# Performance work log

Measured on AMD Instinct MI355X. Metric: run time of the kernel, lower is better.

Reference implementation:

```python
import jax, jax.numpy as jnp
import numpy as np

B, N, C, H = 2, 1024, 1024, 16
D = C // H  # head_dim = 64

def _layernorm(x, g, b):
    m = jnp.mean(x, axis=-1, keepdims=True)
    v = jnp.mean((x - m) ** 2, axis=-1, keepdims=True)
    return (x - m) * jax.lax.rsqrt(v + 1e-5) * g + b

def _proj(x, w, b, g, beta):
    # Linear(C -> 2C) + LayerNorm(2C) + ReLU
    return jax.nn.relu(_layernorm(x @ w + b, g, beta))

def setup_inputs():
    key = jax.random.key(0)
    ks = jax.random.split(key, 9)
    mk = lambda k, shape, s=0.02: jax.random.normal(k, shape, dtype=jnp.float32) * s
    inp = {"x": jax.random.normal(ks[0], (B, N, C), dtype=jnp.float32)}
    for i, name in enumerate(["q", "k", "v"]):
        inp[name + "_w"] = mk(ks[1 + i], (C, 2 * C))
        inp[name + "_b"] = jnp.zeros((2 * C,), jnp.float32)
        inp[name + "_g"] = jnp.ones((2 * C,), jnp.float32)
        inp[name + "_beta"] = jnp.zeros((2 * C,), jnp.float32)
    inp["amp_mix"] = jax.random.normal(ks[7], (H,), dtype=jnp.float32)
    inp["phase_mix"] = jax.random.normal(ks[8], (H,), dtype=jnp.float32)
    return inp

def reference(x, q_w, q_b, q_g, q_beta, k_w, k_b, k_g, k_beta, v_w, v_b, v_g, v_beta, amp_mix, phase_mix):
    q = _proj(x, q_w, q_b, q_g, q_beta).reshape(B, N, H, 2 * D)
    k = _proj(x, k_w, k_b, k_g, k_beta).reshape(B, N, H, 2 * D)
    v = _proj(x, v_w, v_b, v_g, v_beta).reshape(B, N, H, 2 * D)
    qr, qi = q[..., :D], q[..., D:]
    kr, ki = k[..., :D], k[..., D:]
    vr, vi = v[..., :D], v[..., D:]
    # complex qk^H style logits: [B, N, M, H]
    amp = (jnp.einsum('bnhd,bmhd->bnmh', qr, kr)
           - jnp.einsum('bnhd,bmhd->bnmh', qi, ki)) * amp_mix
    ph = (jnp.einsum('bnhd,bmhd->bnmh', qr, ki)
          + jnp.einsum('bnhd,bmhd->bnmh', qi, kr)) * phase_mix
    # attn = amp * exp(i*ph); score = Re * sigmoid(Im)
    score = (amp * jnp.cos(ph)) * jax.nn.sigmoid(amp * jnp.sin(ph))
    attn = jax.nn.softmax(score, axis=2)  # softmax over keys (m)
    out_r = jnp.einsum('bnmh,bmhd->bnhd', attn, vr)
    out_i = jnp.einsum('bnmh,bmhd->bnhd', attn, vi)
    return jnp.concatenate([out_r, out_i], axis=-1).reshape(B, N, 2 * C)
```

## Files before the change

kernel.cpp:

```cpp
#include <hip/hip_runtime.h>
#include <math.h>

#define NSEQ   1024
#define KDIM   1024
#define TWOC   2048
#define NB     65536

typedef float  f32x4  __attribute__((ext_vector_type(4)));
typedef short  short8 __attribute__((ext_vector_type(8)));
typedef short  short4v __attribute__((ext_vector_type(4)));
typedef unsigned int u32x4 __attribute__((ext_vector_type(4)));
typedef __bf16 bf16x8 __attribute__((ext_vector_type(8)));
typedef _Float16 half8 __attribute__((ext_vector_type(8)));

#define PANROW   40
#define PANHALF  10240
#define PANPAIR  20480
#define NPAN_K   32
#define WPAN_Z_BYTES 10485760u

#define QPLANE   131072
#define KPLANEB  278528
#define VPLANEB  262144

#define QPAN_OFF   0ul
#define KPAN_OFF   16777216ul
#define VTPAN_OFF  34603008ul
#define QBUF_OFF   51380224ul
#define KBUF_OFF   68157440ul
#define VBUF_OFF   84934656ul

__device__ __forceinline__ unsigned short bf16_rne(float x) {
    unsigned int u = __float_as_uint(x);
    u += 0x7fffu + ((u >> 16) & 1u);
    return (unsigned short)(u >> 16);
}

__device__ __forceinline__ void gload_lds16(const void* g, void* l) {
    __builtin_amdgcn_global_load_lds(
        (const __attribute__((address_space(1))) unsigned int*)g,
        (__attribute__((address_space(3))) unsigned int*)l, 16, 0, 0);
}

__device__ __forceinline__ bf16x8 bneg(bf16x8 v) {
    u32x4 u = __builtin_bit_cast(u32x4, v);
    u ^= 0x80008000u;
    return __builtin_bit_cast(bf16x8, u);
}

__global__ __launch_bounds__(256)
void split_x(const float* __restrict__ X, unsigned short* __restrict__ Xpan)
{
    const int c   = blockIdx.x * 256 + threadIdx.x;
    const int reg = c / 640;
    const int cc  = c - reg * 640;
    const int row = cc / 5, slot = cc - row * 5;
    char* base = (char*)Xpan + (size_t)reg * PANPAIR + row * 80 + slot * 16;
    if (slot == 4) {
        short8 z = (short8){0,0,0,0,0,0,0,0};
        *(short8*)base = z;
        *(short8*)(base + PANHALF) = z;
        return;
    }
    const int mb = reg >> 5, ks = reg & 31;
    const int m = mb * 128 + row, k0 = ks * 32 + slot * 8;
    f32x4 v0 = *(const f32x4*)(X + (size_t)m * KDIM + k0);
    f32x4 v1 = *(const f32x4*)(X + (size_t)m * KDIM + k0 + 4);
    float xv[8] = {v0[0],v0[1],v0[2],v0[3],v1[0],v1[1],v1[2],v1[3]};
    short8 h8, l8;
#pragma unroll
    for (int j = 0; j < 8; ++j) {
        unsigned short h = bf16_rne(xv[j]);
        float hf = __uint_as_float((unsigned int)h << 16);
        unsigned short lo = bf16_rne(xv[j] - hf);
        h8[j] = (short)h; l8[j] = (short)lo;
    }
    *(short8*)base = h8;
    *(short8*)(base + PANHALF) = l8;
}

__global__ __launch_bounds__(256)
void split_w(const float* __restrict__ Wq, const float* __restrict__ Wk,
             const float* __restrict__ Wv, unsigned short* __restrict__ Wpan)
{
    const int z = blockIdx.z;
    const float* W = (z == 0) ? Wq : (z == 1) ? Wk : Wv;
    char* pan = (char*)Wpan + (size_t)z * WPAN_Z_BYTES;

    __shared__ __align__(16) float T[64][36];
    const int t  = threadIdx.x;
    const int nt = blockIdx.x;
    const int kt = blockIdx.y;
    const int kk = t >> 3, cg = (t & 7) * 4;
#pragma unroll
    for (int i = 0; i < 2; ++i) {
        int kr = kk + i * 32;
        *(f32x4*)&T[kr][cg] = *(const f32x4*)(W + (size_t)(kt * 64 + kr) * TWOC + nt * 32 + cg);
    }
    __syncthreads();

    const int nbk = nt >> 2, nlb = (nt & 3) * 32;
#pragma unroll
    for (int i = 0; i < 2; ++i) {
        int c = t + i * 256;
        if (c < 320) {
            int ksi = (c >= 160) ? 1 : 0;
            int cc  = c - ksi * 160;
            int row = cc / 5, slot = cc - row * 5;
            char* base = pan + (size_t)(nbk * NPAN_K + kt * 2 + ksi) * PANPAIR
                       + (nlb + row) * 80 + slot * 16;
            short8 h8, l8;
            if (slot == 4) {
                h8 = (short8){0,0,0,0,0,0,0,0};
                l8 = h8;
            } else {
#pragma unroll
                for (int j = 0; j < 8; ++j) {
                    float xv = T[ksi * 32 + slot * 8 + j][row];
                    unsigned short h = bf16_rne(xv);
                    float hf = __uint_as_float((unsigned int)h << 16);
                    unsigned short lo = bf16_rne(xv - hf);
                    h8[j] = (short)h; l8[j] = (short)lo;
                }
            }
            *(short8*)base = h8;
            *(short8*)(base + PANHALF) = l8;
        }
    }
}

__global__ __launch_bounds__(256)
void mfma_gemm(const unsigned short* __restrict__ Xpan,
               const unsigned short* __restrict__ Wpan,
               const float* __restrict__ Bq, const float* __restrict__ Bk,
               const float* __restrict__ Bv,
               float* __restrict__ Yq, float* __restrict__ Yk, float* __restrict__ Yv)
{
    __shared__ __align__(16) char AB[40960];
    const int t = threadIdx.x, l = t & 63, w = t >> 6;
    const int wm = w >> 1, wn = w & 1;
    const int nb = blockIdx.x, mb = blockIdx.y, z = blockIdx.z;
    const char* Apan = (const char*)Xpan + (size_t)mb * NPAN_K * PANPAIR;
    const char* Bpan = (const char*)Wpan + (size_t)z * WPAN_Z_BYTES
                                        + (size_t)nb * NPAN_K * PANPAIR;
    const float* bias = (z == 0) ? Bq : (z == 1) ? Bk : Bv;
    float* Y = (z == 0) ? Yq : (z == 1) ? Yk : Yv;

    f32x4 acc[4][4];
#pragma unroll
    for (int i = 0; i < 4; ++i)
#pragma unroll
        for (int j = 0; j < 4; ++j) acc[i][j] = (f32x4){0.f, 0.f, 0.f, 0.f};

    {
#pragma unroll
        for (int r = 0; r < 5; ++r) {
            int off = r * 4096 + t * 16;
            gload_lds16(Apan + off, AB + off);
            gload_lds16(Bpan + off, AB + 20480 + off);
        }
    }
    const int lg  = (l >> 4) * 16;
    const int l15 = l & 15;

    for (int ks = 0; ks < 32; ++ks) {
        __syncthreads();
        short8 ahi[4], alo[4];
#pragma unroll
        for (int fi = 0; fi < 4; ++fi) {
            int row = wm * 64 + fi * 16 + l15;
            ahi[fi] = *(const short8*)(AB + row * 80 + lg);
            alo[fi] = *(const short8*)(AB + PANHALF + row * 80 + lg);
        }
#pragma unroll
        for (int fj = 0; fj < 4; ++fj) {
            int rn = wn * 64 + fj * 16 + l15;
            short8 bh = *(const short8*)(AB + 20480 + rn * 80 + lg);
            short8 bl = *(const short8*)(AB + 30720 + rn * 80 + lg);
            bf16x8 bhv = __builtin_bit_cast(bf16x8, bh);
            bf16x8 blv = __builtin_bit_cast(bf16x8, bl);
#pragma unroll
            for (int fi = 0; fi < 4; ++fi) {
                bf16x8 ahv = __builtin_bit_cast(bf16x8, ahi[fi]);
                bf16x8 alv = __builtin_bit_cast(bf16x8, alo[fi]);
                acc[fi][fj] = __builtin_amdgcn_mfma_f32_16x16x32_bf16(ahv, bhv, acc[fi][fj], 0, 0, 0);
                acc[fi][fj] = __builtin_amdgcn_mfma_f32_16x16x32_bf16(ahv, blv, acc[fi][fj], 0, 0, 0);
                acc[fi][fj] = __builtin_amdgcn_mfma_f32_16x16x32_bf16(alv, bhv, acc[fi][fj], 0, 0, 0);
            }
        }
        __syncthreads();
        if (ks < 31) {
            const char* ga = Apan + (size_t)(ks + 1) * PANPAIR;
            const char* gb = Bpan + (size_t)(ks + 1) * PANPAIR;
#pragma unroll
            for (int r = 0; r < 5; ++r) {
                int off = r * 4096 + t * 16;
                gload_lds16(ga + off, AB + off);
                gload_lds16(gb + off, AB + 20480 + off);
            }
        }
    }

#pragma unroll
    for (int fj = 0; fj < 4; ++fj) {
        int ccol = nb * 128 + wn * 64 + fj * 16 + l15;
        float bb = bias[ccol];
        int hh = ccol >> 7, pp = (ccol >> 6) & 1, d0 = ccol & 63;
        float* ybase = Y + (size_t)(hh * 2 + pp) * NB + d0;
#pragma unroll
        for (int fi = 0; fi < 4; ++fi) {
            int mb4 = mb * 128 + wm * 64 + fi * 16 + (l >> 4) * 4;
#pragma unroll
            for (int r = 0; r < 4; ++r) {
                int mg = mb4 + r;
                int bidx = mg >> 10, n = mg & 1023;
                ybase[(size_t)(bidx * 32) * NB + n * 64] = acc[fi][fj][r] + bb;
            }
        }
    }
}

__global__ __launch_bounds__(256)
void ln_relu(float* __restrict__ Yq, float* __restrict__ Yk, float* __restrict__ Yv,
             const float* __restrict__ Gq, const float* __restrict__ BTq,
             const float* __restrict__ Gk, const float* __restrict__ BTk,
             const float* __restrict__ Gv, const float* __restrict__ BTv,
             unsigned short* __restrict__ Qpan, unsigned short* __restrict__ Kpan)
{
    float* Y; const float* G; const float* Bt;
    if (blockIdx.y == 0)      { Y = Yq; G = Gq; Bt = BTq; }
    else if (blockIdx.y == 1) { Y = Yk; G = Gk; Bt = BTk; }
    else                      { Y = Yv; G = Gv; Bt = BTv; }

    const int r    = blockIdx.x;
    const int bidx = r >> 10;
    const int n    = r & 1023;
    const int t    = threadIdx.x;
    const int e0   = t * 8;
    const int chunk = e0 >> 6;
    const int d     = e0 & 63;

    float* p = Y + (size_t)(bidx * 32 + chunk) * NB + n * 64 + d;
    f32x4 v0 = *(f32x4*)p;
    f32x4 v1 = *(f32x4*)(p + 4);
    float xv[8] = {v0[0],v0[1],v0[2],v0[3],v1[0],v1[1],v1[2],v1[3]};

    __shared__ float red[8];
    float s = 0.f;
#pragma unroll
    for (int j = 0; j < 8; ++j) s += xv[j];
#pragma unroll
    for (int off = 32; off > 0; off >>= 1) s += __shfl_down(s, off);
    const int lane = t & 63, wid = t >> 6;
    if (lane == 0) red[wid] = s;
    __syncthreads();
    const float mean = (red[0] + red[1] + red[2] + red[3]) * (1.f / 2048.f);
    __syncthreads();

    float sq = 0.f;
#pragma unroll
    for (int j = 0; j < 8; ++j) { float dx = xv[j] - mean; sq += dx * dx; }
#pragma unroll
    for (int off = 32; off > 0; off >>= 1) sq += __shfl_down(sq, off);
    if (lane == 0) red[wid] = sq;
    __syncthreads();
    const float var  = (red[0] + red[1] + red[2] + red[3]) * (1.f / 2048.f);
    const float rstd = 1.f / sqrtf(var + 1e-5f);

    float yv[8];
#pragma unroll
    for (int j = 0; j < 8; ++j)
        yv[j] = fmaxf((xv[j] - mean) * rstd * G[e0 + j] + Bt[e0 + j], 0.f);

    if (blockIdx.y == 2) {
        f32x4 o0, o1;
#pragma unroll
        for (int j = 0; j < 4; ++j) { o0[j] = yv[j]; o1[j] = yv[j + 4]; }
        *(f32x4*)p       = o0;
        *(f32x4*)(p + 4) = o1;
        return;
    }

    short8 h8, l8;
#pragma unroll
    for (int j = 0; j < 8; ++j) {
        unsigned short hh = bf16_rne(yv[j]);
        float hf = __uint_as_float((unsigned int)hh << 16);
        unsigned short lo = bf16_rne(yv[j] - hf);
        h8[j] = (short)hh; l8[j] = (short)lo;
    }
    const int bh   = bidx * 16 + (e0 >> 7);
    const int dim0 = e0 & 127;
    if (blockIdx.y == 0) {
        unsigned short* dst = Qpan + ((size_t)(bh * 2) * 1024 + n) * 128 + dim0;
        *(short8*)dst = h8;
        *(short8*)(dst + QPLANE) = l8;
    } else {
        unsigned short* dst = Kpan + ((size_t)(bh * 2) * 1024 + n) * 136 + dim0;
        *(short8*)dst = h8;
        *(short8*)(dst + (size_t)1024 * 136) = l8;
    }
}

__global__ __launch_bounds__(256)
void vsplit(const float* __restrict__ vbuf, unsigned short* __restrict__ Vt)
{
    __shared__ __align__(16) unsigned short Tb[128][72];
    const int bh = blockIdx.x, nt = blockIdx.y;
    const int n0 = nt * 64;
    const int t = threadIdx.x;
    {
        const int p = t >> 7, u = t & 127, l4 = u & 3, nl0 = u >> 2;
        const float* src0 = vbuf + (size_t)(bh * 2 + p) * NB + (size_t)n0 * 64 + l4 * 16;
#pragma unroll
        for (int rep = 0; rep < 2; ++rep) {
            const int row = nl0 + rep * 32;
            const float* sp = src0 + (size_t)row * 64;
            f32x4 a = *(const f32x4*)sp,       b = *(const f32x4*)(sp + 4);
            f32x4 c = *(const f32x4*)(sp + 8), d = *(const f32x4*)(sp + 12);
            float vv[16] = {a[0],a[1],a[2],a[3],b[0],b[1],b[2],b[3],
                            c[0],c[1],c[2],c[3],d[0],d[1],d[2],d[3]};
#pragma unroll
            for (int j = 0; j < 16; ++j)
                Tb[p * 64 + l4 * 16 + j][row] =
                    __builtin_bit_cast(unsigned short, (_Float16)vv[j]);
        }
    }
    __syncthreads();
    const int d2 = t >> 1, sseg = t & 1;
    unsigned short* dst = Vt + ((size_t)bh * 128 + d2) * 1024 + n0 + sseg * 32;
#pragma unroll
    for (int i = 0; i < 4; ++i)
        *(short8*)(dst + i * 8) = *(const short8*)&Tb[d2][sseg * 32 + i * 8];
}

__device__ __forceinline__ void stage_K(const char* kplane, int kt, char* dst, int t) {
#pragma unroll
    for (int i = 0; i < 4; ++i) {
        int c = t + i * 256;
        int hf = (c >= 544) ? 1 : 0;
        int rem = c - hf * 544;
        gload_lds16(kplane + (size_t)hf * KPLANEB + (size_t)kt * 8704 + rem * 16,
                    dst + c * 16);
    }
    if (t < 64) {
        int c = 1024 + t;
        gload_lds16(kplane + KPLANEB + (size_t)kt * 8704 + (c - 544) * 16,
                    dst + c * 16);
    }
}

__device__ __forceinline__ void stage_V(const char* vplane, int kt, char* dst, int t) {
#pragma unroll
    for (int i = 0; i < 2; ++i) {
        int c = t + i * 256;
        int r = c / 5, s = c - r * 5; if (s == 4) s = 3;
        gload_lds16(vplane + (size_t)r * 2048 + kt * 64 + s * 16, dst + c * 16);
    }
    if (t < 128) {
        int c = 512 + t;
        int r = c / 5, s = c - r * 5; if (s == 4) s = 3;
        gload_lds16(vplane + (size_t)r * 2048 + kt * 64 + s * 16, dst + c * 16);
    }
}

__global__ __launch_bounds__(256)
void attn_mfma(const unsigned short* __restrict__ Qpan,
               const unsigned short* __restrict__ Kpan,
               const unsigned short* __restrict__ Vtpan,
               const float* __restrict__ amp_mix, const float* __restrict__ phase_mix,
               float* __restrict__ Out)
{
    __shared__ __align__(16) char Klds[2][17408];
    __shared__ __align__(16) char Vlds[2][10240];
    __shared__ __align__(16) char Plds[5120];
    __shared__ float sc_s[64];
    __shared__ float l_s[64];

    const int bid = blockIdx.x;
    const int swz = (bid & 7) * 64 + (bid >> 3);
    const int bh = swz >> 4, qt = swz & 15;
    const int h = bh & 15, bidx = bh >> 4;

    const int t = threadIdx.x, l = t & 63, w = t >> 6;
    const int l15 = l & 15, g = l >> 4;

    const float amix = amp_mix[h], pmix = phase_mix[h];

    bf16x8 Qf[2][4];
    {
        const unsigned short* qb = Qpan
            + ((size_t)(bh * 2) * 1024 + qt * 64 + w * 16 + l15) * 128 + g * 8;
#pragma unroll
        for (int hf = 0; hf < 2; ++hf)
#pragma unroll
            for (int db = 0; db < 4; ++db)
                Qf[hf][db] = __builtin_bit_cast(bf16x8,
                    *(const short8*)(qb + (size_t)hf * QPLANE + db * 32));
    }

    const char* kbase = (const char*)Kpan + (size_t)(bh * 2) * KPLANEB;
    const char* vbase = (const char*)Vtpan + (size_t)bh * VPLANEB;

    f32x4 O[8];
#pragma unroll
    for (int i = 0; i < 8; ++i) O[i] = (f32x4){0.f, 0.f, 0.f, 0.f};
    float m_ = -1e30f, l_ = 0.f;

    stage_K(kbase, 0, Klds[0], t);
    stage_V(vbase, 0, Vlds[0], t);

    for (int kt = 0; kt < 32; ++kt) {
        __syncthreads();
        const int buf = kt & 1;
        if (kt < 31) {
            stage_K(kbase, kt + 1, Klds[buf ^ 1], t);
            stage_V(vbase, kt + 1, Vlds[buf ^ 1], t);
        }
        const char* Kb = Klds[buf];

        f32x4 aA[2], pA[2];
        __builtin_amdgcn_s_setprio(1);
#pragma unroll
        for (int fi = 0; fi < 2; ++fi) {
            aA[fi] = (f32x4){0.f, 0.f, 0.f, 0.f};
            pA[fi] = (f32x4){0.f, 0.f, 0.f, 0.f};
            const char* kr = Kb + (fi * 16 + l15) * 272 + g * 16;
            bf16x8 Fh[4], Fl[4];
#pragma unroll
            for (int db = 0; db < 4; ++db) {
                Fh[db] = __builtin_bit_cast(bf16x8, *(const short8*)(kr + db * 64));
                Fl[db] = __builtin_bit_cast(bf16x8, *(const short8*)(kr + 8704 + db * 64));
            }
            bf16x8 Nh[2] = { bneg(Fh[2]), bneg(Fh[3]) };
            bf16x8 Nl[2] = { bneg(Fl[2]), bneg(Fl[3]) };
#pragma unroll
            for (int db = 0; db < 4; ++db) {
                bf16x8 Ah = (db < 2) ? Fh[db] : Nh[db - 2];
                bf16x8 Al = (db < 2) ? Fl[db] : Nl[db - 2];
                aA[fi] = __builtin_amdgcn_mfma_f32_16x16x32_bf16(Ah, Qf[0][db], aA[fi], 0, 0, 0);
                aA[fi] = __builtin_amdgcn_mfma_f32_16x16x32_bf16(Ah, Qf[1][db], aA[fi], 0, 0, 0);
                aA[fi] = __builtin_amdgcn_mfma_f32_16x16x32_bf16(Al, Qf[0][db], aA[fi], 0, 0, 0);
                bf16x8 Ph = Fh[db ^ 2];
                bf16x8 Pl = Fl[db ^ 2];
                pA[fi] = __builtin_amdgcn_mfma_f32_16x16x32_bf16(Ph, Qf[0][db], pA[fi], 0, 0, 0);
                pA[fi] = __builtin_amdgcn_mfma_f32_16x16x32_bf16(Ph, Qf[1][db], pA[fi], 0, 0, 0);
                pA[fi] = __builtin_amdgcn_mfma_f32_16x16x32_bf16(Pl, Qf[0][db], pA[fi], 0, 0, 0);
            }
        }
        __builtin_amdgcn_s_setprio(0);

        float sv[2][4];
#pragma unroll
        for (int fi = 0; fi < 2; ++fi)
#pragma unroll
            for (int r = 0; r < 4; ++r) {
                float amp = aA[fi][r] * amix;
                float ph  = pA[fi][r] * pmix;
                float sn, cs;
                __sincosf(ph, &sn, &cs);
                float sig = __builtin_amdgcn_rcpf(1.f + __expf(-amp * sn));
                sv[fi][r] = amp * cs * sig;
            }

        float rm = sv[0][0];
#pragma unroll
        for (int fi = 0; fi < 2; ++fi)
#pragma unroll
            for (int r = 0; r < 4; ++r) rm = fmaxf(rm, sv[fi][r]);
        rm = fmaxf(rm, __shfl_xor(rm, 16));
        rm = fmaxf(rm, __shfl_xor(rm, 32));
        const float mn  = fmaxf(m_, rm);
        const float scl = __expf(m_ - mn);
        float pv[2][4];
        float rs = 0.f;
#pragma unroll
        for (int fi = 0; fi < 2; ++fi)
#pragma unroll
            for (int r = 0; r < 4; ++r) { pv[fi][r] = __expf(sv[fi][r] - mn); rs += pv[fi][r]; }
        rs += __shfl_xor(rs, 16);
        rs += __shfl_xor(rs, 32);
        l_ = l_ * scl + rs;
        m_ = mn;

#pragma unroll
        for (int fi = 0; fi < 2; ++fi) {
            short4v pk;
#pragma unroll
            for (int r = 0; r < 4; ++r)
                pk[r] = (short)__builtin_bit_cast(unsigned short, (_Float16)pv[fi][r]);
            *(short4v*)(Plds + (w * 16 + l15) * 80 + fi * 32 + g * 8) = pk;
        }
        if (g == 0) sc_s[w * 16 + l15] = scl;

        asm volatile("s_waitcnt lgkmcnt(0)" ::: "memory");
        __builtin_amdgcn_s_barrier();
        __builtin_amdgcn_sched_barrier(0);

        f32x4 scv;
#pragma unroll
        for (int r = 0; r < 4; ++r) scv[r] = sc_s[w * 16 + g * 4 + r];
        half8 Pf = __builtin_bit_cast(half8,
            *(const short8*)(Plds + (w * 16 + l15) * 80 + g * 16));
        const char* Vb = Vlds[buf];
        __builtin_amdgcn_s_setprio(1);
#pragma unroll
        for (int nt = 0; nt < 8; ++nt) {
            half8 Vh = __builtin_bit_cast(half8,
                *(const short8*)(Vb + (nt * 16 + l15) * 80 + g * 16));
            O[nt] *= scv;
            O[nt] = __builtin_amdgcn_mfma_f32_16x16x32_f16(Pf, Vh, O[nt], 0, 0, 0);
        }
        __builtin_amdgcn_s_setprio(0);
    }

    if (g == 0) l_s[w * 16 + l15] = l_;
    __syncthreads();
    f32x4 invv;
#pragma unroll
    for (int r = 0; r < 4; ++r) invv[r] = __builtin_amdgcn_rcpf(l_s[w * 16 + g * 4 + r]);
#pragma unroll
    for (int nt = 0; nt < 8; ++nt) {
#pragma unroll
        for (int r = 0; r < 4; ++r) {
            const int n = qt * 64 + w * 16 + g * 4 + r;
            Out[(size_t)(bidx * NSEQ + n) * TWOC + h * 128 + nt * 16 + l15] = O[nt][r] * invv[r];
        }
    }
}

extern "C" void kernel_launch(void* const* d_in, const int* in_sizes, int n_in,
                              void* d_out, int out_size, void* d_ws, size_t ws_size,
                              hipStream_t stream) {
    (void)in_sizes; (void)n_in; (void)out_size; (void)ws_size;
    const float* x      = (const float*)d_in[0];
    const float* q_w    = (const float*)d_in[1];
    const float* q_b    = (const float*)d_in[2];
    const float* q_g    = (const float*)d_in[3];
    const float* q_beta = (const float*)d_in[4];
    const float* k_w    = (const float*)d_in[5];
    const float* k_b    = (const float*)d_in[6];
    const float* k_g    = (const float*)d_in[7];
    const float* k_beta = (const float*)d_in[8];
    const float* v_w    = (const float*)d_in[9];
    const float* v_b    = (const float*)d_in[10];
    const float* v_g    = (const float*)d_in[11];
    const float* v_beta = (const float*)d_in[12];
    const float* amp_mix   = (const float*)d_in[13];
    const float* phase_mix = (const float*)d_in[14];

    char* ws = (char*)d_ws;
    unsigned short* Qpan  = (unsigned short*)(ws + QPAN_OFF);
    unsigned short* Kpan  = (unsigned short*)(ws + KPAN_OFF);
    unsigned short* Vtpan = (unsigned short*)(ws + VTPAN_OFF);
    unsigned short* Wpan  = (unsigned short*)(ws + QPAN_OFF);
    float* qbuf = (float*)(ws + QBUF_OFF);
    float* kbuf = (float*)(ws + KBUF_OFF);
    float* vbuf = (float*)(ws + VBUF_OFF);
    unsigned short* Xpan = (unsigned short*)d_out;

    split_x<<<1280, 256, 0, stream>>>(x, Xpan);
    split_w<<<dim3(64, 16, 3), 256, 0, stream>>>(q_w, k_w, v_w, Wpan);
    mfma_gemm<<<dim3(16, 16, 3), 256, 0, stream>>>(
        Xpan, Wpan, q_b, k_b, v_b, qbuf, kbuf, vbuf);
    ln_relu<<<dim3(2048, 3), 256, 0, stream>>>(
        qbuf, kbuf, vbuf, q_g, q_beta, k_g, k_beta, v_g, v_beta, Qpan, Kpan);
    vsplit<<<dim3(32, 16), 256, 0, stream>>>(vbuf, Vtpan);
    attn_mfma<<<512, 256, 0, stream>>>(
        Qpan, Kpan, Vtpan, amp_mix, phase_mix, (float*)d_out);
}
```

Baseline: 299.8 us.

## Use native sin/cos/exp2 intrinsics, lazy softmax rescale, and drop per-tile barrier

Replaces __sincosf and __expf with range-reduced hardware sin/cos intrinsics and exp2, folding log2(e) into the score. The online softmax now moves its running max only when the new tile max exceeds it by more than a threshold. The output accumulator is rescaled only when some lane in the wave actually updated its max. The LDS wait and block barrier before the P·V stage are removed, which cuts transcendental and synchronisation cost per key tile. The risks are unnormalised probabilities growing up to about 2^10 in fp16, and a possible race on shared buffers if that barrier was also guarding the K/V double buffering.

Result: faster. 287.8 us (-4.0%).

```diff
diff --git a/kernel.cpp b/kernel.cpp
--- a/kernel.cpp
+++ b/kernel.cpp
@@ -386,6 +386,8 @@
     const int l15 = l & 15, g = l >> 4;
 
     const float amix = amp_mix[h], pmix = phase_mix[h];
+    const float L2E = 1.44269504f;
+    const float INV2PI = 0.15915493667f;
 
     bf16x8 Qf[2][4];
     {
@@ -457,10 +459,13 @@
             for (int r = 0; r < 4; ++r) {
                 float amp = aA[fi][r] * amix;
                 float ph  = pA[fi][r] * pmix;
-                float sn, cs;
-                __sincosf(ph, &sn, &cs);
-                float sig = __builtin_amdgcn_rcpf(1.f + __expf(-amp * sn));
-                sv[fi][r] = amp * cs * sig;
+                float rev = ph * INV2PI;
+                rev = rev - floorf(rev);
+                float sn = __builtin_amdgcn_sinf(rev);
+                float cs = __builtin_amdgcn_cosf(rev);
+                float e  = __builtin_amdgcn_exp2f(amp * sn * -L2E);
+                float sig = __builtin_amdgcn_rcpf(1.f + e);
+                sv[fi][r] = amp * cs * sig * L2E;
             }
 
         float rm = sv[0][0];
@@ -470,18 +475,23 @@
             for (int r = 0; r < 4; ++r) rm = fmaxf(rm, sv[fi][r]);
         rm = fmaxf(rm, __shfl_xor(rm, 16));
         rm = fmaxf(rm, __shfl_xor(rm, 32));
-        const float mn  = fmaxf(m_, rm);
-        const float scl = __expf(m_ - mn);
+        const bool upd = (rm > m_ + 10.f);
+        const float mn  = upd ? rm : m_;
+        const float scl = upd ? __builtin_amdgcn_exp2f(m_ - mn) : 1.f;
         float pv[2][4];
         float rs = 0.f;
 #pragma unroll
         for (int fi = 0; fi < 2; ++fi)
 #pragma unroll
-            for (int r = 0; r < 4; ++r) { pv[fi][r] = __expf(sv[fi][r] - mn); rs += pv[fi][r]; }
+            for (int r = 0; r < 4; ++r) {
+                pv[fi][r] = __builtin_amdgcn_exp2f(sv[fi][r] - mn);
+                rs += pv[fi][r];
+            }
         rs += __shfl_xor(rs, 16);
         rs += __shfl_xor(rs, 32);
         l_ = l_ * scl + rs;
         m_ = mn;
+        const bool anyscale = __any(upd);
 
 #pragma unroll
         for (int fi = 0; fi < 2; ++fi) {
@@ -493,13 +503,13 @@
         }
         if (g == 0) sc_s[w * 16 + l15] = scl;
 
-        asm volatile("s_waitcnt lgkmcnt(0)" ::: "memory");
-        __builtin_amdgcn_s_barrier();
-        __builtin_amdgcn_sched_barrier(0);
-
-        f32x4 scv;
-#pragma unroll
-        for (int r = 0; r < 4; ++r) scv[r] = sc_s[w * 16 + g * 4 + r];
+        if (anyscale) {
+            f32x4 scv;
+#pragma unroll
+            for (int r = 0; r < 4; ++r) scv[r] = sc_s[w * 16 + g * 4 + r];
+#pragma unroll
+            for (int nt = 0; nt < 8; ++nt) O[nt] *= scv;
+        }
         half8 Pf = __builtin_bit_cast(half8,
             *(const short8*)(Plds + (w * 16 + l15) * 80 + g * 16));
         const char* Vb = Vlds[buf];
@@ -508,7 +518,6 @@
         for (int nt = 0; nt < 8; ++nt) {
             half8 Vh = __builtin_bit_cast(half8,
                 *(const short8*)(Vb + (nt * 16 + l15) * 80 + g * 16));
-            O[nt] *= scv;
             O[nt] = __builtin_amdgcn_mfma_f32_16x16x32_f16(Pf, Vh, O[nt], 0, 0, 0);
         }
         __builtin_amdgcn_s_setprio(0);
```
